# Optimization experiments

Hardware: AMD Instinct MI355X
Metric: run time of the kernel (lower is better)

## Reference

```python
import jax, jax.numpy as jnp
import numpy as np
import math

B, T, D = 2, 2048, 1024
NH, DH = 16, 64
MLP = 4096


def setup_inputs() -> dict:
    key = jax.random.key(0)
    ks = jax.random.split(key, 10)
    xavier = lambda k, shape: jax.random.uniform(
        k, shape, jnp.float32,
        -math.sqrt(6.0 / (shape[0] + shape[1])), math.sqrt(6.0 / (shape[0] + shape[1])))
    return {
        "inputs": jax.random.normal(ks[0], (B, T, D), jnp.float32),
        "cond": jax.random.normal(ks[1], (B, D), jnp.float32),
        "attention_mask": jnp.zeros((T, T), jnp.bool_),
        # LayerNorm params
        "ln1_g": jnp.ones((D,), jnp.float32), "ln1_b": jnp.zeros((D,), jnp.float32),
        "ln2_g": jnp.ones((D,), jnp.float32), "ln2_b": jnp.zeros((D,), jnp.float32),
        # Attention params (torch Linear stores weight as [out,in]; we store [in,out])
        "w_qkv": xavier(ks[2], (D, 3 * D)),
        "w_out": xavier(ks[3], (D, D)),
        "b_out": jax.random.normal(ks[4], (D,), jnp.float32),
        # MLP params
        "w1": xavier(ks[5], (D, MLP)), "b1": jax.random.normal(ks[6], (MLP,), jnp.float32),
        "w2": xavier(ks[7], (MLP, D)), "b2": jax.random.normal(ks[8], (D,), jnp.float32),
    }


def layer_norm(x, g, b, eps=1e-5):
    mu = jnp.mean(x, axis=-1, keepdims=True)
    var = jnp.var(x, axis=-1, keepdims=True)
    return (x - mu) * jax.lax.rsqrt(var + eps) * g + b


def reference(inputs, cond, attention_mask, ln1_g, ln1_b, ln2_g, ln2_b,
              w_qkv, w_out, b_out, w1, b1, w2, b2):
    # del cond, attention_mask  (unused in use_rs_attn path)
    x = layer_norm(inputs, ln1_g, ln1_b)
    qkv = x @ w_qkv  # [B,T,3D]
    q, k, v = jnp.split(qkv, 3, axis=-1)
    # [B,T,D] -> [B,NH,T,DH]
    split_heads = lambda t: t.reshape(B, T, NH, DH).transpose(0, 2, 1, 3)
    q, k, v = split_heads(q), split_heads(k), split_heads(v)
    att = jnp.einsum('bhqd,bhkd->bhqk', q, k) * (1.0 / math.sqrt(DH))
    att = jax.nn.softmax(att, axis=-1)  # NOTE: no causal mask in original
    y = jnp.einsum('bhqk,bhkd->bhqd', att, v)
    y = y.transpose(0, 2, 1, 3).reshape(B, T, D)
    y = y @ w_out + b_out
    x = y + inputs  # residual (dropout = identity in eval)
    h = layer_norm(x, ln2_g, ln2_b)
    h = jax.nn.gelu(h @ w1 + b1, approximate=False)
    h = h @ w2 + b2
    return x + h
```

## Files before the change

### kernel.cpp

```cpp
#include <hip/hip_runtime.h>
#include <hip/hip_bf16.h>
#include <math.h>

using bf16 = __hip_bfloat16;
typedef __attribute__((ext_vector_type(8))) short bf16x8;
typedef __attribute__((ext_vector_type(4))) float f32x4;

#define B_   2
#define T_   2048
#define D_   1024
#define NH_  16
#define DH_  64
#define MLP_ 4096
#define ROWS (B_ * T_)
#define BHTD ((size_t)32 * 2048 * 64)

__global__ void wtrans_kernel(const float* __restrict__ W, bf16* __restrict__ Wt,
                              int K, int N) {
    __shared__ float tile[32][33];
    int n0 = blockIdx.x * 32, k0 = blockIdx.y * 32;
    int tx = threadIdx.x, ty = threadIdx.y;
#pragma unroll
    for (int i = 0; i < 32; i += 8)
        tile[ty + i][tx] = W[(size_t)(k0 + ty + i) * N + n0 + tx];
    __syncthreads();
#pragma unroll
    for (int i = 0; i < 32; i += 8)
        Wt[(size_t)(n0 + ty + i) * K + k0 + tx] = __float2bfloat16(tile[tx][ty + i]);
}

__global__ void transpose_v_kernel(const bf16* __restrict__ V, bf16* __restrict__ Vt) {
    __shared__ bf16 tile[32][33];
    int bh = blockIdx.z;
    int t0 = blockIdx.x * 32;
    int d0 = blockIdx.y * 32;
    int tx = threadIdx.x, ty = threadIdx.y;
    const bf16* src = V + (size_t)bh * T_ * 64;
    bf16* dst = Vt + (size_t)bh * 64 * T_;
#pragma unroll
    for (int i = 0; i < 32; i += 8)
        tile[ty + i][tx] = src[(size_t)(t0 + ty + i) * 64 + d0 + tx];
    __syncthreads();
#pragma unroll
    for (int i = 0; i < 32; i += 8)
        dst[(size_t)(d0 + ty + i) * T_ + t0 + tx] = tile[tx][ty + i];
}

__global__ void ln_kernel(const float* __restrict__ x, const float* __restrict__ g,
                          const float* __restrict__ bta, bf16* __restrict__ out) {
    int row = blockIdx.x;
    int t = threadIdx.x;
    float4 v = ((const float4*)(x + (size_t)row * D_))[t];
    float s1 = v.x + v.y + v.z + v.w;
    float s2 = v.x * v.x + v.y * v.y + v.z * v.z + v.w * v.w;
#pragma unroll
    for (int m = 1; m < 64; m <<= 1) {
        s1 += __shfl_xor(s1, m);
        s2 += __shfl_xor(s2, m);
    }
    __shared__ float red[8];
    int wid = t >> 6, lane = t & 63;
    if (lane == 0) { red[wid] = s1; red[4 + wid] = s2; }
    __syncthreads();
    s1 = red[0] + red[1] + red[2] + red[3];
    s2 = red[4] + red[5] + red[6] + red[7];
    float mu = s1 * (1.0f / D_);
    float var = s2 * (1.0f / D_) - mu * mu;
    float rs = rsqrtf(var + 1e-5f);
    float4 gv = ((const float4*)g)[t];
    float4 bv = ((const float4*)bta)[t];
    bf16* o = out + (size_t)row * D_ + t * 4;
    o[0] = __float2bfloat16((v.x - mu) * rs * gv.x + bv.x);
    o[1] = __float2bfloat16((v.y - mu) * rs * gv.y + bv.y);
    o[2] = __float2bfloat16((v.z - mu) * rs * gv.z + bv.z);
    o[3] = __float2bfloat16((v.w - mu) * rs * gv.w + bv.w);
}

template <int EPI>
__global__ __launch_bounds__(256) void gemm_bt(const bf16* __restrict__ A,
                                               const bf16* __restrict__ Bt,
                                               int N, int K,
                                               const float* __restrict__ bias,
                                               const float* __restrict__ resid,
                                               void* __restrict__ out) {
    __shared__ __align__(16) bf16 Asm[128][72];
    __shared__ __align__(16) bf16 Bsm[128][72];
    int tid = threadIdx.x;
    int bm = blockIdx.y * 128;
    int bn = blockIdx.x * 128;
    int wid = tid >> 6, lane = tid & 63;
    int wr = wid >> 1, wc = wid & 1;
    f32x4 acc[4][4];
#pragma unroll
    for (int m = 0; m < 4; m++)
#pragma unroll
        for (int n = 0; n < 4; n++) acc[m][n] = (f32x4){0.f, 0.f, 0.f, 0.f};

    for (int k0 = 0; k0 < K; k0 += 64) {
        __syncthreads();
#pragma unroll
        for (int i = 0; i < 4; i++) {
            int c = tid + i * 256;
            int row = c >> 3, col8 = (c & 7) * 8;
            *(uint4*)&Asm[row][col8] = *(const uint4*)&A[(size_t)(bm + row) * K + k0 + col8];
            *(uint4*)&Bsm[row][col8] = *(const uint4*)&Bt[(size_t)(bn + row) * K + k0 + col8];
        }
        __syncthreads();
#pragma unroll
        for (int kk = 0; kk < 2; kk++) {
            bf16x8 af[4], bfr[4];
#pragma unroll
            for (int m = 0; m < 4; m++)
                af[m] = *(const bf16x8*)&Asm[wr * 64 + m * 16 + (lane & 15)][kk * 32 + (lane >> 4) * 8];
#pragma unroll
            for (int n = 0; n < 4; n++)
                bfr[n] = *(const bf16x8*)&Bsm[wc * 64 + n * 16 + (lane & 15)][kk * 32 + (lane >> 4) * 8];
#pragma unroll
            for (int m = 0; m < 4; m++)
#pragma unroll
                for (int n = 0; n < 4; n++)
                    acc[m][n] = __builtin_amdgcn_mfma_f32_16x16x32_bf16(af[m], bfr[n], acc[m][n], 0, 0, 0);
        }
    }
    int r0 = bm + wr * 64;
    int c0 = bn + wc * 64;
#pragma unroll
    for (int m = 0; m < 4; m++) {
#pragma unroll
        for (int n = 0; n < 4; n++) {
#pragma unroll
            for (int j = 0; j < 4; j++) {
                int r = r0 + m * 16 + (lane >> 4) * 4 + j;
                int c = c0 + n * 16 + (lane & 15);
                float v = acc[m][n][j];
                if constexpr (EPI == 0) {
                    int which = c >> 10, d = c & 1023;
                    int h = d >> 6, dh = d & 63;
                    int b = r >> 11, t = r & 2047;
                    ((bf16*)out)[(((size_t)which * 32 + b * 16 + h) * 2048 + t) * 64 + dh] =
                        __float2bfloat16(v);
                } else if constexpr (EPI == 1) {
                    ((float*)out)[(size_t)r * N + c] = v + bias[c] + resid[(size_t)r * N + c];
                } else {
                    float u = v + bias[c];
                    float ge = 0.5f * u * (1.0f + erff(u * 0.70710678118f));
                    ((bf16*)out)[(size_t)r * N + c] = __float2bfloat16(ge);
                }
            }
        }
    }
}

__global__ __launch_bounds__(256) void attn_kernel(const bf16* __restrict__ Q,
                                                   const bf16* __restrict__ Kt,
                                                   const bf16* __restrict__ Vt,
                                                   bf16* __restrict__ Y) {
    __shared__ __align__(16) bf16 Ksm[64][72];
    __shared__ __align__(16) bf16 Vsm[64][72];
    __shared__ __align__(16) bf16 Psm[4][16][72];
    int tid = threadIdx.x;
    int wid = tid >> 6, lane = tid & 63;
    int bh = blockIdx.y;
    int q0 = blockIdx.x * 64 + wid * 16;
    const bf16* Qb = Q + (size_t)bh * T_ * 64;
    const bf16* Kb = Kt + (size_t)bh * T_ * 64;
    const bf16* Vb = Vt + (size_t)bh * 64 * T_;

    bf16x8 aq[2];
#pragma unroll
    for (int kk = 0; kk < 2; kk++)
        aq[kk] = *(const bf16x8*)&Qb[(size_t)(q0 + (lane & 15)) * 64 + kk * 32 + (lane >> 4) * 8];

    float mrow[4], lrow[4];
    f32x4 o[4];
#pragma unroll
    for (int j = 0; j < 4; j++) { mrow[j] = -1e30f; lrow[j] = 0.f; }
#pragma unroll
    for (int n = 0; n < 4; n++) o[n] = (f32x4){0.f, 0.f, 0.f, 0.f};

    for (int kt = 0; kt < T_ / 64; kt++) {
        __syncthreads();
#pragma unroll
        for (int i = 0; i < 2; i++) {
            int c = tid + i * 256;
            int row = c >> 3, col8 = (c & 7) * 8;
            *(uint4*)&Ksm[row][col8] = *(const uint4*)&Kb[(size_t)(kt * 64 + row) * 64 + col8];
            *(uint4*)&Vsm[row][col8] = *(const uint4*)&Vb[(size_t)row * T_ + kt * 64 + col8];
        }
        __syncthreads();

        f32x4 s[4];
#pragma unroll
        for (int n = 0; n < 4; n++) {
            bf16x8 b0 = *(const bf16x8*)&Ksm[n * 16 + (lane & 15)][(lane >> 4) * 8];
            bf16x8 b1 = *(const bf16x8*)&Ksm[n * 16 + (lane & 15)][32 + (lane >> 4) * 8];
            s[n] = __builtin_amdgcn_mfma_f32_16x16x32_bf16(aq[0], b0, (f32x4){0.f, 0.f, 0.f, 0.f}, 0, 0, 0);
            s[n] = __builtin_amdgcn_mfma_f32_16x16x32_bf16(aq[1], b1, s[n], 0, 0, 0);
        }
#pragma unroll
        for (int n = 0; n < 4; n++) s[n] *= 0.125f;

        float mnew[4], sc[4];
#pragma unroll
        for (int j = 0; j < 4; j++) {
            float mj = fmaxf(fmaxf(s[0][j], s[1][j]), fmaxf(s[2][j], s[3][j]));
            mj = fmaxf(mj, __shfl_xor(mj, 1));
            mj = fmaxf(mj, __shfl_xor(mj, 2));
            mj = fmaxf(mj, __shfl_xor(mj, 4));
            mj = fmaxf(mj, __shfl_xor(mj, 8));
            float mn = fmaxf(mrow[j], mj);
            sc[j] = __expf(mrow[j] - mn);
            mnew[j] = mn;
            mrow[j] = mn;
        }
        float psum[4] = {0.f, 0.f, 0.f, 0.f};
#pragma unroll
        for (int n = 0; n < 4; n++)
#pragma unroll
            for (int j = 0; j < 4; j++) {
                float pv = __expf(s[n][j] - mnew[j]);
                s[n][j] = pv;
                psum[j] += pv;
            }
#pragma unroll
        for (int j = 0; j < 4; j++) {
            psum[j] += __shfl_xor(psum[j], 1);
            psum[j] += __shfl_xor(psum[j], 2);
            psum[j] += __shfl_xor(psum[j], 4);
            psum[j] += __shfl_xor(psum[j], 8);
            lrow[j] = lrow[j] * sc[j] + psum[j];
        }
#pragma unroll
        for (int n = 0; n < 4; n++)
#pragma unroll
            for (int j = 0; j < 4; j++) o[n][j] *= sc[j];

#pragma unroll
        for (int n = 0; n < 4; n++)
#pragma unroll
            for (int j = 0; j < 4; j++)
                Psm[wid][(lane >> 4) * 4 + j][n * 16 + (lane & 15)] = __float2bfloat16(s[n][j]);

        bf16x8 pa[2];
#pragma unroll
        for (int kk = 0; kk < 2; kk++)
            pa[kk] = *(const bf16x8*)&Psm[wid][lane & 15][kk * 32 + (lane >> 4) * 8];

#pragma unroll
        for (int n = 0; n < 4; n++) {
            bf16x8 v0 = *(const bf16x8*)&Vsm[n * 16 + (lane & 15)][(lane >> 4) * 8];
            bf16x8 v1 = *(const bf16x8*)&Vsm[n * 16 + (lane & 15)][32 + (lane >> 4) * 8];
            o[n] = __builtin_amdgcn_mfma_f32_16x16x32_bf16(pa[0], v0, o[n], 0, 0, 0);
            o[n] = __builtin_amdgcn_mfma_f32_16x16x32_bf16(pa[1], v1, o[n], 0, 0, 0);
        }
    }

    int b = bh >> 4, h = bh & 15;
#pragma unroll
    for (int j = 0; j < 4; j++) {
        float inv = 1.0f / lrow[j];
        int t = q0 + (lane >> 4) * 4 + j;
#pragma unroll
        for (int n = 0; n < 4; n++) {
            int c = h * 64 + n * 16 + (lane & 15);
            Y[((size_t)b * T_ + t) * D_ + c] = __float2bfloat16(o[n][j] * inv);
        }
    }
}

extern "C" void kernel_launch(void* const* d_in, const int* in_sizes, int n_in,
                              void* d_out, int out_size, void* d_ws, size_t ws_size,
                              hipStream_t stream) {
    const float* inputs = (const float*)d_in[0];
    const float* ln1_g = (const float*)d_in[3];
    const float* ln1_b = (const float*)d_in[4];
    const float* ln2_g = (const float*)d_in[5];
    const float* ln2_b = (const float*)d_in[6];
    const float* w_qkv = (const float*)d_in[7];
    const float* w_out = (const float*)d_in[8];
    const float* b_out = (const float*)d_in[9];
    const float* w1    = (const float*)d_in[10];
    const float* b1    = (const float*)d_in[11];
    const float* w2    = (const float*)d_in[12];
    const float* b2    = (const float*)d_in[13];

    char* p = (char*)d_ws;
    auto alloc = [&](size_t bytes) {
        void* r = (void*)p;
        p += (bytes + 255) & ~(size_t)255;
        return r;
    };
    bf16* x1     = (bf16*)alloc((size_t)ROWS * D_ * 2);
    bf16* wqkv_t = (bf16*)alloc((size_t)3 * D_ * D_ * 2);
    bf16* wout_t = (bf16*)alloc((size_t)D_ * D_ * 2);
    bf16* w1_t   = (bf16*)alloc((size_t)MLP_ * D_ * 2);
    bf16* w2_t   = (bf16*)alloc((size_t)D_ * MLP_ * 2);
    bf16* qkv    = (bf16*)alloc((size_t)3 * BHTD * 2);
    bf16* vt     = (bf16*)alloc((size_t)BHTD * 2);
    bf16* y      = (bf16*)alloc((size_t)ROWS * D_ * 2);
    float* x2    = (float*)alloc((size_t)ROWS * D_ * 4);
    bf16* h2     = (bf16*)alloc((size_t)ROWS * D_ * 2);
    bf16* act    = (bf16*)alloc((size_t)ROWS * MLP_ * 2);

    dim3 tb(32, 8);
    wtrans_kernel<<<dim3(3 * D_ / 32, D_ / 32), tb, 0, stream>>>(w_qkv, wqkv_t, D_, 3 * D_);
    wtrans_kernel<<<dim3(D_ / 32, D_ / 32), tb, 0, stream>>>(w_out, wout_t, D_, D_);
    wtrans_kernel<<<dim3(MLP_ / 32, D_ / 32), tb, 0, stream>>>(w1, w1_t, D_, MLP_);
    wtrans_kernel<<<dim3(D_ / 32, MLP_ / 32), tb, 0, stream>>>(w2, w2_t, MLP_, D_);

    ln_kernel<<<ROWS, 256, 0, stream>>>(inputs, ln1_g, ln1_b, x1);

    gemm_bt<0><<<dim3(3 * D_ / 128, ROWS / 128), 256, 0, stream>>>(
        x1, wqkv_t, 3 * D_, D_, nullptr, nullptr, (void*)qkv);

    transpose_v_kernel<<<dim3(T_ / 32, 2, 32), tb, 0, stream>>>(qkv + 2 * BHTD, vt);

    attn_kernel<<<dim3(T_ / 64, 32), 256, 0, stream>>>(qkv, qkv + BHTD, vt, y);

    gemm_bt<1><<<dim3(D_ / 128, ROWS / 128), 256, 0, stream>>>(
        y, wout_t, D_, D_, b_out, inputs, (void*)x2);

    ln_kernel<<<ROWS, 256, 0, stream>>>(x2, ln2_g, ln2_b, h2);

    gemm_bt<2><<<dim3(MLP_ / 128, ROWS / 128), 256, 0, stream>>>(
        h2, w1_t, MLP_, D_, b1, nullptr, (void*)act);

    gemm_bt<1><<<dim3(D_ / 128, ROWS / 128), 256, 0, stream>>>(
        act, w2_t, D_, MLP_, b2, x2, d_out);
}
```

Measured before the change: 480.5 us.

## Use direct global-to-LDS loads in GEMM and widen attention key tiles

The GEMM now stages A and B tiles with global_load_lds, which writes global memory straight into LDS without going through registers, and drops the row padding to do so. This removes the padding that avoided LDS bank conflicts, so the fragment reads may now conflict. The attention kernel processes 128 keys per iteration instead of 64, halving the number of barriers and loop iterations at the cost of more registers and LDS. It also folds log2(e) into the score scale so it can use exp2f instead of __expf.

```diff
diff --git a/kernel.cpp b/kernel.cpp
--- a/kernel.cpp
+++ b/kernel.cpp
@@ -14,6 +14,12 @@
 #define MLP_ 4096
 #define ROWS (B_ * T_)
 #define BHTD ((size_t)32 * 2048 * 64)
+
+__device__ __forceinline__ void gload_lds16(const void* g, void* l) {
+    __builtin_amdgcn_global_load_lds(
+        (const __attribute__((address_space(1))) unsigned int*)g,
+        (__attribute__((address_space(3))) unsigned int*)l, 16, 0, 0);
+}
 
 __global__ void wtrans_kernel(const float* __restrict__ W, bf16* __restrict__ Wt,
                               int K, int N) {
@@ -83,8 +89,8 @@
                                                const float* __restrict__ bias,
                                                const float* __restrict__ resid,
                                                void* __restrict__ out) {
-    __shared__ __align__(16) bf16 Asm[128][72];
-    __shared__ __align__(16) bf16 Bsm[128][72];
+    __shared__ __align__(16) bf16 Asm[128 * 64];
+    __shared__ __align__(16) bf16 Bsm[128 * 64];
     int tid = threadIdx.x;
     int bm = blockIdx.y * 128;
     int bn = blockIdx.x * 128;
@@ -102,8 +108,8 @@
         for (int i = 0; i < 4; i++) {
             int c = tid + i * 256;
             int row = c >> 3, col8 = (c & 7) * 8;
-            *(uint4*)&Asm[row][col8] = *(const uint4*)&A[(size_t)(bm + row) * K + k0 + col8];
-            *(uint4*)&Bsm[row][col8] = *(const uint4*)&Bt[(size_t)(bn + row) * K + k0 + col8];
+            gload_lds16(&A[(size_t)(bm + row) * K + k0 + col8], &Asm[c * 8]);
+            gload_lds16(&Bt[(size_t)(bn + row) * K + k0 + col8], &Bsm[c * 8]);
         }
         __syncthreads();
 #pragma unroll
@@ -111,10 +117,10 @@
             bf16x8 af[4], bfr[4];
 #pragma unroll
             for (int m = 0; m < 4; m++)
-                af[m] = *(const bf16x8*)&Asm[wr * 64 + m * 16 + (lane & 15)][kk * 32 + (lane >> 4) * 8];
+                af[m] = *(const bf16x8*)&Asm[(wr * 64 + m * 16 + (lane & 15)) * 64 + kk * 32 + (lane >> 4) * 8];
 #pragma unroll
             for (int n = 0; n < 4; n++)
-                bfr[n] = *(const bf16x8*)&Bsm[wc * 64 + n * 16 + (lane & 15)][kk * 32 + (lane >> 4) * 8];
+                bfr[n] = *(const bf16x8*)&Bsm[(wc * 64 + n * 16 + (lane & 15)) * 64 + kk * 32 + (lane >> 4) * 8];
 #pragma unroll
             for (int m = 0; m < 4; m++)
 #pragma unroll
@@ -151,13 +157,14 @@
     }
 }
 
+#define SCL 0.18033688011112042f
 __global__ __launch_bounds__(256) void attn_kernel(const bf16* __restrict__ Q,
                                                    const bf16* __restrict__ Kt,
                                                    const bf16* __restrict__ Vt,
                                                    bf16* __restrict__ Y) {
-    __shared__ __align__(16) bf16 Ksm[64][72];
-    __shared__ __align__(16) bf16 Vsm[64][72];
-    __shared__ __align__(16) bf16 Psm[4][16][72];
+    __shared__ __align__(16) bf16 Ksm[128][72];
+    __shared__ __align__(16) bf16 Vsm[64][136];
+    __shared__ __align__(16) bf16 Psm[4][16][136];
     int tid = threadIdx.x;
     int wid = tid >> 6, lane = tid & 63;
     int bh = blockIdx.y;
@@ -178,47 +185,53 @@
 #pragma unroll
     for (int n = 0; n < 4; n++) o[n] = (f32x4){0.f, 0.f, 0.f, 0.f};
 
-    for (int kt = 0; kt < T_ / 64; kt++) {
+    for (int kt = 0; kt < T_ / 128; kt++) {
         __syncthreads();
 #pragma unroll
-        for (int i = 0; i < 2; i++) {
+        for (int i = 0; i < 4; i++) {
             int c = tid + i * 256;
             int row = c >> 3, col8 = (c & 7) * 8;
-            *(uint4*)&Ksm[row][col8] = *(const uint4*)&Kb[(size_t)(kt * 64 + row) * 64 + col8];
-            *(uint4*)&Vsm[row][col8] = *(const uint4*)&Vb[(size_t)row * T_ + kt * 64 + col8];
+            *(uint4*)&Ksm[row][col8] = *(const uint4*)&Kb[(size_t)(kt * 128 + row) * 64 + col8];
+        }
+#pragma unroll
+        for (int i = 0; i < 4; i++) {
+            int c = tid + i * 256;
+            int row = c >> 4, col8 = (c & 15) * 8;
+            *(uint4*)&Vsm[row][col8] = *(const uint4*)&Vb[(size_t)row * T_ + kt * 128 + col8];
         }
         __syncthreads();
 
-        f32x4 s[4];
-#pragma unroll
-        for (int n = 0; n < 4; n++) {
+        f32x4 s[8];
+#pragma unroll
+        for (int n = 0; n < 8; n++) {
             bf16x8 b0 = *(const bf16x8*)&Ksm[n * 16 + (lane & 15)][(lane >> 4) * 8];
             bf16x8 b1 = *(const bf16x8*)&Ksm[n * 16 + (lane & 15)][32 + (lane >> 4) * 8];
             s[n] = __builtin_amdgcn_mfma_f32_16x16x32_bf16(aq[0], b0, (f32x4){0.f, 0.f, 0.f, 0.f}, 0, 0, 0);
             s[n] = __builtin_amdgcn_mfma_f32_16x16x32_bf16(aq[1], b1, s[n], 0, 0, 0);
         }
 #pragma unroll
-        for (int n = 0; n < 4; n++) s[n] *= 0.125f;
+        for (int n = 0; n < 8; n++) s[n] *= SCL;
 
         float mnew[4], sc[4];
 #pragma unroll
         for (int j = 0; j < 4; j++) {
-            float mj = fmaxf(fmaxf(s[0][j], s[1][j]), fmaxf(s[2][j], s[3][j]));
+            float mj = fmaxf(fmaxf(fmaxf(s[0][j], s[1][j]), fmaxf(s[2][j], s[3][j])),
+                             fmaxf(fmaxf(s[4][j], s[5][j]), fmaxf(s[6][j], s[7][j])));
             mj = fmaxf(mj, __shfl_xor(mj, 1));
             mj = fmaxf(mj, __shfl_xor(mj, 2));
             mj = fmaxf(mj, __shfl_xor(mj, 4));
             mj = fmaxf(mj, __shfl_xor(mj, 8));
             float mn = fmaxf(mrow[j], mj);
-            sc[j] = __expf(mrow[j] - mn);
+            sc[j] = exp2f(mrow[j] - mn);
             mnew[j] = mn;
             mrow[j] = mn;
         }
         float psum[4] = {0.f, 0.f, 0.f, 0.f};
 #pragma unroll
-        for (int n = 0; n < 4; n++)
+        for (int n = 0; n < 8; n++)
 #pragma unroll
             for (int j = 0; j < 4; j++) {
-                float pv = __expf(s[n][j] - mnew[j]);
+                float pv = exp2f(s[n][j] - mnew[j]);
                 s[n][j] = pv;
                 psum[j] += pv;
             }
@@ -236,22 +249,23 @@
             for (int j = 0; j < 4; j++) o[n][j] *= sc[j];
 
 #pragma unroll
-        for (int n = 0; n < 4; n++)
+        for (int n = 0; n < 8; n++)
 #pragma unroll
             for (int j = 0; j < 4; j++)
                 Psm[wid][(lane >> 4) * 4 + j][n * 16 + (lane & 15)] = __float2bfloat16(s[n][j]);
 
-        bf16x8 pa[2];
-#pragma unroll
-        for (int kk = 0; kk < 2; kk++)
+        bf16x8 pa[4];
+#pragma unroll
+        for (int kk = 0; kk < 4; kk++)
             pa[kk] = *(const bf16x8*)&Psm[wid][lane & 15][kk * 32 + (lane >> 4) * 8];
 
 #pragma unroll
         for (int n = 0; n < 4; n++) {
-            bf16x8 v0 = *(const bf16x8*)&Vsm[n * 16 + (lane & 15)][(lane >> 4) * 8];
-            bf16x8 v1 = *(const bf16x8*)&Vsm[n * 16 + (lane & 15)][32 + (lane >> 4) * 8];
-            o[n] = __builtin_amdgcn_mfma_f32_16x16x32_bf16(pa[0], v0, o[n], 0, 0, 0);
-            o[n] = __builtin_amdgcn_mfma_f32_16x16x32_bf16(pa[1], v1, o[n], 0, 0, 0);
+#pragma unroll
+            for (int ks = 0; ks < 4; ks++) {
+                bf16x8 v = *(const bf16x8*)&Vsm[n * 16 + (lane & 15)][ks * 32 + (lane >> 4) * 8];
+                o[n] = __builtin_amdgcn_mfma_f32_16x16x32_bf16(pa[ks], v, o[n], 0, 0, 0);
+            }
         }
     }
 
```

Result: slower. 546.8 us (+13.8%).

## Use direct global-to-LDS loads, tile swizzle in GEMM, larger attention blocks with exp2

Applied to the files above, without the earlier changes.

The GEMM now loads A and B tiles straight into LDS with global_load_lds, which bypasses registers, and drops the row padding. It also remaps workgroup IDs so neighbouring blocks share tiles in L2. The attention kernel doubles to 512 threads and 128 query rows per block, halving K/V tile reloads, and folds log2(e) into the scale so it can use exp2f. The unpadded LDS layout may add bank conflicts on the fragment reads, and fewer, larger attention blocks lower grid parallelism.

```diff
diff --git a/kernel.cpp b/kernel.cpp
--- a/kernel.cpp
+++ b/kernel.cpp
@@ -14,6 +14,12 @@
 #define MLP_ 4096
 #define ROWS (B_ * T_)
 #define BHTD ((size_t)32 * 2048 * 64)
+
+__device__ __forceinline__ void gload_lds16(const void* g, void* l) {
+    __builtin_amdgcn_global_load_lds(
+        (const __attribute__((address_space(1))) unsigned int*)g,
+        (__attribute__((address_space(3))) unsigned int*)l, 16, 0, 0);
+}
 
 __global__ void wtrans_kernel(const float* __restrict__ W, bf16* __restrict__ Wt,
                               int K, int N) {
@@ -83,11 +89,14 @@
                                                const float* __restrict__ bias,
                                                const float* __restrict__ resid,
                                                void* __restrict__ out) {
-    __shared__ __align__(16) bf16 Asm[128][72];
-    __shared__ __align__(16) bf16 Bsm[128][72];
+    __shared__ __align__(16) bf16 Asm[128 * 64];
+    __shared__ __align__(16) bf16 Bsm[128 * 64];
     int tid = threadIdx.x;
-    int bm = blockIdx.y * 128;
-    int bn = blockIdx.x * 128;
+    int nwg = gridDim.x * gridDim.y;
+    int wg = blockIdx.y * gridDim.x + blockIdx.x;
+    int swz = (wg & 7) * (nwg >> 3) + (wg >> 3);
+    int bm = (swz / gridDim.x) * 128;
+    int bn = (swz % gridDim.x) * 128;
     int wid = tid >> 6, lane = tid & 63;
     int wr = wid >> 1, wc = wid & 1;
     f32x4 acc[4][4];
@@ -102,8 +111,8 @@
         for (int i = 0; i < 4; i++) {
             int c = tid + i * 256;
             int row = c >> 3, col8 = (c & 7) * 8;
-            *(uint4*)&Asm[row][col8] = *(const uint4*)&A[(size_t)(bm + row) * K + k0 + col8];
-            *(uint4*)&Bsm[row][col8] = *(const uint4*)&Bt[(size_t)(bn + row) * K + k0 + col8];
+            gload_lds16(&A[(size_t)(bm + row) * K + k0 + col8], &Asm[c * 8]);
+            gload_lds16(&Bt[(size_t)(bn + row) * K + k0 + col8], &Bsm[c * 8]);
         }
         __syncthreads();
 #pragma unroll
@@ -111,10 +120,10 @@
             bf16x8 af[4], bfr[4];
 #pragma unroll
             for (int m = 0; m < 4; m++)
-                af[m] = *(const bf16x8*)&Asm[wr * 64 + m * 16 + (lane & 15)][kk * 32 + (lane >> 4) * 8];
+                af[m] = *(const bf16x8*)&Asm[(wr * 64 + m * 16 + (lane & 15)) * 64 + kk * 32 + (lane >> 4) * 8];
 #pragma unroll
             for (int n = 0; n < 4; n++)
-                bfr[n] = *(const bf16x8*)&Bsm[wc * 64 + n * 16 + (lane & 15)][kk * 32 + (lane >> 4) * 8];
+                bfr[n] = *(const bf16x8*)&Bsm[(wc * 64 + n * 16 + (lane & 15)) * 64 + kk * 32 + (lane >> 4) * 8];
 #pragma unroll
             for (int m = 0; m < 4; m++)
 #pragma unroll
@@ -151,17 +160,18 @@
     }
 }
 
-__global__ __launch_bounds__(256) void attn_kernel(const bf16* __restrict__ Q,
+#define SCL 0.18033688011112042f
+__global__ __launch_bounds__(512) void attn_kernel(const bf16* __restrict__ Q,
                                                    const bf16* __restrict__ Kt,
                                                    const bf16* __restrict__ Vt,
                                                    bf16* __restrict__ Y) {
     __shared__ __align__(16) bf16 Ksm[64][72];
     __shared__ __align__(16) bf16 Vsm[64][72];
-    __shared__ __align__(16) bf16 Psm[4][16][72];
+    __shared__ __align__(16) bf16 Psm[8][16][72];
     int tid = threadIdx.x;
     int wid = tid >> 6, lane = tid & 63;
     int bh = blockIdx.y;
-    int q0 = blockIdx.x * 64 + wid * 16;
+    int q0 = blockIdx.x * 128 + wid * 16;
     const bf16* Qb = Q + (size_t)bh * T_ * 64;
     const bf16* Kb = Kt + (size_t)bh * T_ * 64;
     const bf16* Vb = Vt + (size_t)bh * 64 * T_;
@@ -180,10 +190,8 @@
 
     for (int kt = 0; kt < T_ / 64; kt++) {
         __syncthreads();
-#pragma unroll
-        for (int i = 0; i < 2; i++) {
-            int c = tid + i * 256;
-            int row = c >> 3, col8 = (c & 7) * 8;
+        {
+            int row = tid >> 3, col8 = (tid & 7) * 8;
             *(uint4*)&Ksm[row][col8] = *(const uint4*)&Kb[(size_t)(kt * 64 + row) * 64 + col8];
             *(uint4*)&Vsm[row][col8] = *(const uint4*)&Vb[(size_t)row * T_ + kt * 64 + col8];
         }
@@ -198,7 +206,7 @@
             s[n] = __builtin_amdgcn_mfma_f32_16x16x32_bf16(aq[1], b1, s[n], 0, 0, 0);
         }
 #pragma unroll
-        for (int n = 0; n < 4; n++) s[n] *= 0.125f;
+        for (int n = 0; n < 4; n++) s[n] *= SCL;
 
         float mnew[4], sc[4];
 #pragma unroll
@@ -209,7 +217,7 @@
             mj = fmaxf(mj, __shfl_xor(mj, 4));
             mj = fmaxf(mj, __shfl_xor(mj, 8));
             float mn = fmaxf(mrow[j], mj);
-            sc[j] = __expf(mrow[j] - mn);
+            sc[j] = exp2f(mrow[j] - mn);
             mnew[j] = mn;
             mrow[j] = mn;
         }
@@ -218,7 +226,7 @@
         for (int n = 0; n < 4; n++)
 #pragma unroll
             for (int j = 0; j < 4; j++) {
-                float pv = __expf(s[n][j] - mnew[j]);
+                float pv = exp2f(s[n][j] - mnew[j]);
                 s[n][j] = pv;
                 psum[j] += pv;
             }
@@ -315,7 +323,7 @@
 
     transpose_v_kernel<<<dim3(T_ / 32, 2, 32), tb, 0, stream>>>(qkv + 2 * BHTD, vt);
 
-    attn_kernel<<<dim3(T_ / 64, 32), 256, 0, stream>>>(qkv, qkv + BHTD, vt, y);
+    attn_kernel<<<dim3(T_ / 128, 32), 512, 0, stream>>>(qkv, qkv + BHTD, vt, y);
 
     gemm_bt<1><<<dim3(D_ / 128, ROWS / 128), 256, 0, stream>>>(
         y, wout_t, D_, D_, b_out, inputs, (void*)x2);
```

Result: slower. 505.8 us (+5.3%).
